# Kernel optimization log

Hardware: AMD Instinct MI355X
Metric: run time of the kernel (lower is better)

The kernel has to match this reference:

```python
import jax, jax.numpy as jnp
import numpy as np

N = 100000
E = 1600000
IN_DIM, HID_DIM, OUT_DIM = 128, 128, 64


def setup_inputs() -> dict:
    key = jax.random.key(0)
    k1, k2, k3, k4, k5, k6 = jax.random.split(key, 6)
    x = jax.random.normal(k1, (N, IN_DIM), dtype=jnp.float32)
    edge_index = jax.random.randint(k2, (2, E), 0, N, dtype=jnp.int64)
    # Glorot-style scaled weights (PyG GCNConv: Linear without bias + separate bias)
    W1 = jax.random.normal(k3, (IN_DIM, HID_DIM), dtype=jnp.float32) / np.sqrt(IN_DIM)
    b1 = jnp.zeros((HID_DIM,), dtype=jnp.float32)
    W2 = jax.random.normal(k4, (HID_DIM, OUT_DIM), dtype=jnp.float32) / np.sqrt(HID_DIM)
    b2 = jnp.zeros((OUT_DIM,), dtype=jnp.float32)
    return {"x": x, "W1": W1, "b1": b1, "W2": W2, "b2": b2, "edge_index": edge_index}


def _gcn_norm(edge_index, num_nodes):
    """Add self-loops and compute symmetric normalization D^-1/2 A_hat D^-1/2."""
    loop = jnp.arange(num_nodes, dtype=edge_index.dtype)
    src = jnp.concatenate([edge_index[0], loop])  # [E + N]
    dst = jnp.concatenate([edge_index[1], loop])
    deg = jax.ops.segment_sum(jnp.ones_like(dst, dtype=jnp.float32), dst,
                              num_segments=num_nodes)
    deg_inv_sqrt = jnp.where(deg > 0, jax.lax.rsqrt(deg), 0.0)
    norm = deg_inv_sqrt[src] * deg_inv_sqrt[dst]  # [E + N]
    return src, dst, norm


def _gcn_conv(x, W, b, src, dst, norm, num_nodes):
    h = x @ W                                   # [N, out]  dense transform first
    msg = norm[:, None] * h[src]                # gather + scale over edges
    out = jax.ops.segment_sum(msg, dst, num_segments=num_nodes)  # scatter-add
    return out + b


def reference(x, W1, b1, W2, b2, edge_index):
    num_nodes = x.shape[0]
    src, dst, norm = _gcn_norm(edge_index, num_nodes)
    h = jax.nn.relu(_gcn_conv(x, W1, b1, src, dst, norm, num_nodes))
    out = _gcn_conv(h, W2, b2, src, dst, norm, num_nodes)
    return out
```

## Files before the change

### kernel.cpp

```cpp
#include <hip/hip_runtime.h>

#define NODES 100000
#define EDGES 1600000
#define CHUNK 8192
#define NCH 196
#define BSH 9
#define NBUCK 196

typedef unsigned int uint;
typedef unsigned short ushort;

__device__ __forceinline__ float bf2f(uint u) {
    union { uint i; float f; } c; c.i = u << 16; return c.f;
}
__device__ __forceinline__ ushort f2bf(float f) {
    union { float f; uint i; } c; c.f = f;
    uint r = c.i + 0x7fff + ((c.i >> 16) & 1);
    return (ushort)(r >> 16);
}


__global__ __launch_bounds__(256) void k_hist(const int* __restrict__ dst,
                                              int* __restrict__ hist) {
    __shared__ int h[NBUCK];
    const int t = threadIdx.x;
    if (t < NBUCK) h[t] = 0;
    __syncthreads();
    const int base = blockIdx.x * CHUNK;
    const int len = min(CHUNK, EDGES - base);
    for (int i = t; i < len; i += 256)
        atomicAdd(&h[dst[base + i] >> BSH], 1);
    __syncthreads();
    if (t < NBUCK) hist[blockIdx.x * NBUCK + t] = h[t];
}

__global__ void k_offsets(int* __restrict__ hist, int* __restrict__ bucketStart,
                          int* __restrict__ rowptr) {
    __shared__ int tot[NBUCK];
    __shared__ int bstart[NBUCK + 1];
    const int t = threadIdx.x;
    if (t < NBUCK) {
        int run = 0;
        for (int blk = 0; blk < NCH; ++blk) {
            int c = hist[blk * NBUCK + t];
            hist[blk * NBUCK + t] = run;
            run += c;
        }
        tot[t] = run;
    }
    __syncthreads();
    if (t == 0) {
        int acc = 0;
        for (int b = 0; b < NBUCK; ++b) { bstart[b] = acc; acc += tot[b]; }
        bstart[NBUCK] = acc;
        rowptr[NODES] = acc;
    }
    __syncthreads();
    if (t < NBUCK) {
        int bs = bstart[t];
        for (int blk = 0; blk < NCH; ++blk)
            hist[blk * NBUCK + t] += bs;
    }
    if (t <= NBUCK) bucketStart[t] = bstart[t];
}

__global__ __launch_bounds__(256) void k_bin(const int* __restrict__ src,
                                             const int* __restrict__ dst,
                                             const int* __restrict__ hist,
                                             uint* __restrict__ binned) {
    __shared__ int curs[NBUCK];
    const int t = threadIdx.x;
    if (t < NBUCK) curs[t] = hist[blockIdx.x * NBUCK + t];
    __syncthreads();
    const int base = blockIdx.x * CHUNK;
    const int len = min(CHUNK, EDGES - base);
    for (int i = t; i < len; i += 256) {
        int d = dst[base + i];
        int s = src[base + i];
        int pos = atomicAdd(&curs[d >> BSH], 1);
        binned[pos] = ((uint)(d & 511) << 17) | (uint)s;
    }
}

__global__ __launch_bounds__(256) void k_build(const uint* __restrict__ binned,
                                               const int* __restrict__ bucketStart,
                                               int* __restrict__ rowptr,
                                               float* __restrict__ dis,
                                               int* __restrict__ ssrc) {
    __shared__ int cnt[512];
    __shared__ int sh[256];
    const int t = threadIdx.x;
    const int b = blockIdx.x;
    const int eBase = bucketStart[b], eEnd = bucketStart[b + 1];
    const int nodeBase = b << BSH;
    const int nnode = min(512, NODES - nodeBase);
    cnt[t * 2] = 0; cnt[t * 2 + 1] = 0;
    __syncthreads();
    for (int i = eBase + t; i < eEnd; i += 256)
        atomicAdd(&cnt[binned[i] >> 17], 1);
    __syncthreads();
    const int c0 = cnt[t * 2], c1 = cnt[t * 2 + 1];
    const int sum = c0 + c1;
    sh[t] = sum; __syncthreads();
    for (int off = 1; off < 256; off <<= 1) {
        int add = (t >= off) ? sh[t - off] : 0;
        __syncthreads(); sh[t] += add; __syncthreads();
    }
    int excl = sh[t] - sum;
    const int ln0 = t * 2;
    if (ln0 < nnode) {
        rowptr[nodeBase + ln0] = eBase + excl;
        dis[nodeBase + ln0] = rsqrtf((float)(1 + c0));
    }
    int excl1 = excl + c0;
    if (ln0 + 1 < nnode) {
        rowptr[nodeBase + ln0 + 1] = eBase + excl1;
        dis[nodeBase + ln0 + 1] = rsqrtf((float)(1 + c1));
    }
    cnt[ln0] = excl; cnt[ln0 + 1] = excl1;
    __syncthreads();
    for (int i = eBase + t; i < eEnd; i += 256) {
        uint p = binned[i];
        int pos = atomicAdd(&cnt[p >> 17], 1);
        ssrc[eBase + pos] = (int)(p & 0x1FFFFu);
    }
}


__global__ __launch_bounds__(256) void k_gemm1(const float* __restrict__ x,
                                               const float* __restrict__ W1,
                                               const float* __restrict__ dis,
                                               ushort* __restrict__ hb) {
    __shared__ float wsh[128 * 128];
    __shared__ float xs[32 * 128];
    const int t = threadIdx.x;
    {
        const float4* Wv = (const float4*)W1;
        float4* Sv = (float4*)wsh;
#pragma unroll
        for (int i = 0; i < 16; ++i) Sv[i * 256 + t] = Wv[i * 256 + t];
    }
    const int row0 = blockIdx.x * 32;
    {
        const float4* Xv = (const float4*)(x + (size_t)row0 * 128);
        float4* Sv = (float4*)xs;
#pragma unroll
        for (int i = 0; i < 4; ++i) Sv[i * 256 + t] = Xv[i * 256 + t];
    }
    __syncthreads();
    const int c4 = (t & 31) * 4;
    const int r0 = (t >> 5) * 4;
    float4 a0{0,0,0,0}, a1{0,0,0,0}, a2{0,0,0,0}, a3{0,0,0,0};
#pragma unroll 4
    for (int k = 0; k < 128; ++k) {
        float4 w = *(const float4*)&wsh[k * 128 + c4];
        float x0 = xs[(r0 + 0) * 128 + k];
        float x1 = xs[(r0 + 1) * 128 + k];
        float x2 = xs[(r0 + 2) * 128 + k];
        float x3 = xs[(r0 + 3) * 128 + k];
        a0.x = fmaf(x0, w.x, a0.x); a0.y = fmaf(x0, w.y, a0.y);
        a0.z = fmaf(x0, w.z, a0.z); a0.w = fmaf(x0, w.w, a0.w);
        a1.x = fmaf(x1, w.x, a1.x); a1.y = fmaf(x1, w.y, a1.y);
        a1.z = fmaf(x1, w.z, a1.z); a1.w = fmaf(x1, w.w, a1.w);
        a2.x = fmaf(x2, w.x, a2.x); a2.y = fmaf(x2, w.y, a2.y);
        a2.z = fmaf(x2, w.z, a2.z); a2.w = fmaf(x2, w.w, a2.w);
        a3.x = fmaf(x3, w.x, a3.x); a3.y = fmaf(x3, w.y, a3.y);
        a3.z = fmaf(x3, w.z, a3.z); a3.w = fmaf(x3, w.w, a3.w);
    }
    const float d0 = dis[row0 + r0], d1 = dis[row0 + r0 + 1];
    const float d2 = dis[row0 + r0 + 2], d3 = dis[row0 + r0 + 3];
    size_t base = (size_t)(row0 + r0) * 128 + c4;
    ushort4 u;
    u.x = f2bf(a0.x * d0); u.y = f2bf(a0.y * d0); u.z = f2bf(a0.z * d0); u.w = f2bf(a0.w * d0);
    *(ushort4*)&hb[base] = u;
    u.x = f2bf(a1.x * d1); u.y = f2bf(a1.y * d1); u.z = f2bf(a1.z * d1); u.w = f2bf(a1.w * d1);
    *(ushort4*)&hb[base + 128] = u;
    u.x = f2bf(a2.x * d2); u.y = f2bf(a2.y * d2); u.z = f2bf(a2.z * d2); u.w = f2bf(a2.w * d2);
    *(ushort4*)&hb[base + 256] = u;
    u.x = f2bf(a3.x * d3); u.y = f2bf(a3.y * d3); u.z = f2bf(a3.z * d3); u.w = f2bf(a3.w * d3);
    *(ushort4*)&hb[base + 384] = u;
}

__global__ __launch_bounds__(256) void k_gemm2(const uint* __restrict__ ab,
                                               const float* __restrict__ W2,
                                               const float* __restrict__ dis,
                                               ushort* __restrict__ gb) {
    __shared__ float wsh[128 * 64];
    __shared__ float xs[32 * 132];
    const int t = threadIdx.x;
    {
        const float4* Wv = (const float4*)W2;
        float4* Sv = (float4*)wsh;
#pragma unroll
        for (int i = 0; i < 8; ++i) Sv[i * 256 + t] = Wv[i * 256 + t];
    }
    const int row0 = blockIdx.x * 32;
    {
        const uint4* Xv = (const uint4*)(ab + (size_t)row0 * 64);
#pragma unroll
        for (int i = 0; i < 2; ++i) {
            int f = i * 256 + t;
            uint4 vv = Xv[f];
            int row = f >> 4, col = (f & 15) * 8;
            float* d = &xs[row * 132 + col];
            d[0] = bf2f(vv.x & 0xffffu); d[1] = bf2f(vv.x >> 16);
            d[2] = bf2f(vv.y & 0xffffu); d[3] = bf2f(vv.y >> 16);
            d[4] = bf2f(vv.z & 0xffffu); d[5] = bf2f(vv.z >> 16);
            d[6] = bf2f(vv.w & 0xffffu); d[7] = bf2f(vv.w >> 16);
        }
    }
    __syncthreads();
    const int c4 = (t & 15) * 4;
    const int r0 = (t >> 4) * 2;
    float4 a0{0,0,0,0}, a1{0,0,0,0};
#pragma unroll 4
    for (int k = 0; k < 128; ++k) {
        float4 w = *(const float4*)&wsh[k * 64 + c4];
        float x0 = xs[(r0 + 0) * 132 + k];
        float x1 = xs[(r0 + 1) * 132 + k];
        a0.x = fmaf(x0, w.x, a0.x); a0.y = fmaf(x0, w.y, a0.y);
        a0.z = fmaf(x0, w.z, a0.z); a0.w = fmaf(x0, w.w, a0.w);
        a1.x = fmaf(x1, w.x, a1.x); a1.y = fmaf(x1, w.y, a1.y);
        a1.z = fmaf(x1, w.z, a1.z); a1.w = fmaf(x1, w.w, a1.w);
    }
    const float d0 = dis[row0 + r0], d1 = dis[row0 + r0 + 1];
    size_t base = (size_t)(row0 + r0) * 64 + c4;
    ushort4 u;
    u.x = f2bf(a0.x * d0); u.y = f2bf(a0.y * d0); u.z = f2bf(a0.z * d0); u.w = f2bf(a0.w * d0);
    *(ushort4*)&gb[base] = u;
    u.x = f2bf(a1.x * d1); u.y = f2bf(a1.y * d1); u.z = f2bf(a1.z * d1); u.w = f2bf(a1.w * d1);
    *(ushort4*)&gb[base + 64] = u;
}


__global__ void k_agg1(const int* __restrict__ rowptr, const int* __restrict__ ssrc,
                       const float* __restrict__ dis, const uint2* __restrict__ hb2,
                       const float* __restrict__ b1, uint2* __restrict__ ab2) {
    const int t = threadIdx.x;
    const int lane = t & 63;
    const int q = lane & 31;
    const int v = blockIdx.x * 8 + ((t >> 6) << 1) + (lane >> 5);
    float4 accA, accB = {0.f, 0.f, 0.f, 0.f};
    {
        uint2 pv = hb2[(size_t)v * 32 + q];
        accA.x = bf2f(pv.x & 0xffffu); accA.y = bf2f(pv.x >> 16);
        accA.z = bf2f(pv.y & 0xffffu); accA.w = bf2f(pv.y >> 16);
    }
    int e = rowptr[v];
    const int end = rowptr[v + 1];
    while (e < end) {
        int m = end - e; if (m > 32) m = 32;
        int s = (q < m) ? ssrc[e + q] : 0;
        int i = 0;
        for (; i + 4 <= m; i += 4) {
            int s0 = __shfl(s, i + 0, 32);
            int s1 = __shfl(s, i + 1, 32);
            int s2 = __shfl(s, i + 2, 32);
            int s3 = __shfl(s, i + 3, 32);
            uint2 p0 = hb2[(size_t)s0 * 32 + q];
            uint2 p1 = hb2[(size_t)s1 * 32 + q];
            uint2 p2 = hb2[(size_t)s2 * 32 + q];
            uint2 p3 = hb2[(size_t)s3 * 32 + q];
            accA.x += bf2f(p0.x & 0xffffu); accA.y += bf2f(p0.x >> 16);
            accA.z += bf2f(p0.y & 0xffffu); accA.w += bf2f(p0.y >> 16);
            accB.x += bf2f(p1.x & 0xffffu); accB.y += bf2f(p1.x >> 16);
            accB.z += bf2f(p1.y & 0xffffu); accB.w += bf2f(p1.y >> 16);
            accA.x += bf2f(p2.x & 0xffffu); accA.y += bf2f(p2.x >> 16);
            accA.z += bf2f(p2.y & 0xffffu); accA.w += bf2f(p2.y >> 16);
            accB.x += bf2f(p3.x & 0xffffu); accB.y += bf2f(p3.x >> 16);
            accB.z += bf2f(p3.y & 0xffffu); accB.w += bf2f(p3.y >> 16);
        }
        for (; i < m; ++i) {
            int s0 = __shfl(s, i, 32);
            uint2 p0 = hb2[(size_t)s0 * 32 + q];
            accA.x += bf2f(p0.x & 0xffffu); accA.y += bf2f(p0.x >> 16);
            accA.z += bf2f(p0.y & 0xffffu); accA.w += bf2f(p0.y >> 16);
        }
        e += m;
    }
    const float dv = dis[v];
    const float4 bb = ((const float4*)b1)[q];
    float ox = fmaxf(fmaf(dv, accA.x + accB.x, bb.x), 0.f);
    float oy = fmaxf(fmaf(dv, accA.y + accB.y, bb.y), 0.f);
    float oz = fmaxf(fmaf(dv, accA.z + accB.z, bb.z), 0.f);
    float ow = fmaxf(fmaf(dv, accA.w + accB.w, bb.w), 0.f);
    uint2 o;
    o.x = ((uint)f2bf(oy) << 16) | (uint)f2bf(ox);
    o.y = ((uint)f2bf(ow) << 16) | (uint)f2bf(oz);
    ab2[(size_t)v * 32 + q] = o;
}

__global__ void k_agg2(const int* __restrict__ rowptr, const int* __restrict__ ssrc,
                       const float* __restrict__ dis, const uint* __restrict__ gbu,
                       const float* __restrict__ b2, float* __restrict__ out) {
    const int t = threadIdx.x;
    const int lane = t & 63;
    const int q = lane & 31;
    const int v = blockIdx.x * 8 + ((t >> 6) << 1) + (lane >> 5);
    float2 accA, accB = {0.f, 0.f};
    {
        uint pv = gbu[(size_t)v * 32 + q];
        accA.x = bf2f(pv & 0xffffu); accA.y = bf2f(pv >> 16);
    }
    int e = rowptr[v];
    const int end = rowptr[v + 1];
    while (e < end) {
        int m = end - e; if (m > 32) m = 32;
        int s = (q < m) ? ssrc[e + q] : 0;
        int i = 0;
        for (; i + 4 <= m; i += 4) {
            int s0 = __shfl(s, i + 0, 32);
            int s1 = __shfl(s, i + 1, 32);
            int s2 = __shfl(s, i + 2, 32);
            int s3 = __shfl(s, i + 3, 32);
            uint p0 = gbu[(size_t)s0 * 32 + q];
            uint p1 = gbu[(size_t)s1 * 32 + q];
            uint p2 = gbu[(size_t)s2 * 32 + q];
            uint p3 = gbu[(size_t)s3 * 32 + q];
            accA.x += bf2f(p0 & 0xffffu); accA.y += bf2f(p0 >> 16);
            accB.x += bf2f(p1 & 0xffffu); accB.y += bf2f(p1 >> 16);
            accA.x += bf2f(p2 & 0xffffu); accA.y += bf2f(p2 >> 16);
            accB.x += bf2f(p3 & 0xffffu); accB.y += bf2f(p3 >> 16);
        }
        for (; i < m; ++i) {
            int s0 = __shfl(s, i, 32);
            uint p0 = gbu[(size_t)s0 * 32 + q];
            accA.x += bf2f(p0 & 0xffffu); accA.y += bf2f(p0 >> 16);
        }
        e += m;
    }
    const float dv = dis[v];
    const float2 bb = ((const float2*)b2)[q];
    float2 o;
    o.x = fmaf(dv, accA.x + accB.x, bb.x);
    o.y = fmaf(dv, accA.y + accB.y, bb.y);
    ((float2*)out)[(size_t)v * 32 + q] = o;
}


extern "C" void kernel_launch(void* const* d_in, const int* in_sizes, int n_in,
                              void* d_out, int out_size, void* d_ws, size_t ws_size,
                              hipStream_t stream) {
    const float* x  = (const float*)d_in[0];
    const float* W1 = (const float*)d_in[1];
    const float* b1 = (const float*)d_in[2];
    const float* W2 = (const float*)d_in[3];
    const float* b2 = (const float*)d_in[4];
    const int*   ei = (const int*)d_in[5];
    const int* src = ei;
    const int* dst = ei + EDGES;
    float* out = (float*)d_out;

    char* w = (char*)d_ws;
    int*    hist   = (int*)w;    w += (size_t)NCH * NBUCK * 4 + 256;
    int*    bstart = (int*)w;    w += 256 * 4;
    int*    rowptr = (int*)w;    w += 100004 * 4;
    float*  dis    = (float*)w;  w += 100000 * 4 + 16;
    uint*   binned = (uint*)w;   w += (size_t)EDGES * 4;
    int*    ssrc   = (int*)w;    w += (size_t)EDGES * 4;
    ushort* hb     = (ushort*)w; w += (size_t)NODES * 128 * 2;
    uint*   ab     = (uint*)w;   w += (size_t)NODES * 64 * 4;
    ushort* gb     = (ushort*)w; w += (size_t)NODES * 64 * 2;

    k_hist   <<<NCH, 256, 0, stream>>>(dst, hist);
    k_offsets<<<1, 256, 0, stream>>>(hist, bstart, rowptr);
    k_bin    <<<NCH, 256, 0, stream>>>(src, dst, hist, binned);
    k_build  <<<NBUCK, 256, 0, stream>>>(binned, bstart, rowptr, dis, ssrc);

    k_gemm1  <<<NODES / 32, 256, 0, stream>>>(x, W1, dis, hb);
    k_agg1   <<<NODES / 8, 256, 0, stream>>>(rowptr, ssrc, dis, (const uint2*)hb, b1, (uint2*)ab);
    k_gemm2  <<<NODES / 32, 256, 0, stream>>>(ab, W2, dis, gb);
    k_agg2   <<<NODES / 8, 256, 0, stream>>>(rowptr, ssrc, dis, (const uint*)gb, b2, out);
}
```

Before: 386.0 us.

## Split aggregation feature dimension across blocks for cache locality

Both aggregation kernels now run as grid-stride loops in which each block owns a fixed slice of the feature dimension: 16 features in layer 1, 8 in layer 2. Each wave handles one node at a time, with several edge slots in flight; partial sums are combined by a cross-lane xor-shuffle reduction and one lane group writes the result. The aim is to shrink the per-block gather working set to one slice of the feature table so it stays in L2, and to have more independent edge gathers in flight per wave. The cost is that rowptr and ssrc are re-read once per feature slice, and each gather is a narrow 32- or 16-byte segment rather than a full row.

```diff
diff --git a/kernel.cpp b/kernel.cpp
--- a/kernel.cpp
+++ b/kernel.cpp
@@ -6,6 +6,7 @@
 #define NCH 196
 #define BSH 9
 #define NBUCK 196
+#define NGRP (NODES / 4)
 
 typedef unsigned int uint;
 typedef unsigned short ushort;
@@ -233,108 +234,92 @@
 }
 
 
-__global__ void k_agg1(const int* __restrict__ rowptr, const int* __restrict__ ssrc,
-                       const float* __restrict__ dis, const uint2* __restrict__ hb2,
-                       const float* __restrict__ b1, uint2* __restrict__ ab2) {
-    const int t = threadIdx.x;
+__global__ __launch_bounds__(256) void k_agg1(const int* __restrict__ rowptr,
+                                              const int* __restrict__ ssrc,
+                                              const float* __restrict__ dis,
+                                              const uint* __restrict__ hbu,
+                                              const float* __restrict__ b1,
+                                              uint* __restrict__ abu) {
+    const int t = threadIdx.x;
+    const int wave = t >> 6;
     const int lane = t & 63;
-    const int q = lane & 31;
-    const int v = blockIdx.x * 8 + ((t >> 6) << 1) + (lane >> 5);
-    float4 accA, accB = {0.f, 0.f, 0.f, 0.f};
-    {
-        uint2 pv = hb2[(size_t)v * 32 + q];
-        accA.x = bf2f(pv.x & 0xffffu); accA.y = bf2f(pv.x >> 16);
-        accA.z = bf2f(pv.y & 0xffffu); accA.w = bf2f(pv.y >> 16);
-    }
-    int e = rowptr[v];
-    const int end = rowptr[v + 1];
-    while (e < end) {
-        int m = end - e; if (m > 32) m = 32;
-        int s = (q < m) ? ssrc[e + q] : 0;
-        int i = 0;
-        for (; i + 4 <= m; i += 4) {
-            int s0 = __shfl(s, i + 0, 32);
-            int s1 = __shfl(s, i + 1, 32);
-            int s2 = __shfl(s, i + 2, 32);
-            int s3 = __shfl(s, i + 3, 32);
-            uint2 p0 = hb2[(size_t)s0 * 32 + q];
-            uint2 p1 = hb2[(size_t)s1 * 32 + q];
-            uint2 p2 = hb2[(size_t)s2 * 32 + q];
-            uint2 p3 = hb2[(size_t)s3 * 32 + q];
-            accA.x += bf2f(p0.x & 0xffffu); accA.y += bf2f(p0.x >> 16);
-            accA.z += bf2f(p0.y & 0xffffu); accA.w += bf2f(p0.y >> 16);
-            accB.x += bf2f(p1.x & 0xffffu); accB.y += bf2f(p1.x >> 16);
-            accB.z += bf2f(p1.y & 0xffffu); accB.w += bf2f(p1.y >> 16);
-            accA.x += bf2f(p2.x & 0xffffu); accA.y += bf2f(p2.x >> 16);
-            accA.z += bf2f(p2.y & 0xffffu); accA.w += bf2f(p2.y >> 16);
-            accB.x += bf2f(p3.x & 0xffffu); accB.y += bf2f(p3.x >> 16);
-            accB.z += bf2f(p3.y & 0xffffu); accB.w += bf2f(p3.y >> 16);
-        }
-        for (; i < m; ++i) {
-            int s0 = __shfl(s, i, 32);
-            uint2 p0 = hb2[(size_t)s0 * 32 + q];
-            accA.x += bf2f(p0.x & 0xffffu); accA.y += bf2f(p0.x >> 16);
-            accA.z += bf2f(p0.y & 0xffffu); accA.w += bf2f(p0.y >> 16);
-        }
-        e += m;
-    }
-    const float dv = dis[v];
-    const float4 bb = ((const float4*)b1)[q];
-    float ox = fmaxf(fmaf(dv, accA.x + accB.x, bb.x), 0.f);
-    float oy = fmaxf(fmaf(dv, accA.y + accB.y, bb.y), 0.f);
-    float oz = fmaxf(fmaf(dv, accA.z + accB.z, bb.z), 0.f);
-    float ow = fmaxf(fmaf(dv, accA.w + accB.w, bb.w), 0.f);
-    uint2 o;
-    o.x = ((uint)f2bf(oy) << 16) | (uint)f2bf(ox);
-    o.y = ((uint)f2bf(ow) << 16) | (uint)f2bf(oz);
-    ab2[(size_t)v * 32 + q] = o;
-}
-
-__global__ void k_agg2(const int* __restrict__ rowptr, const int* __restrict__ ssrc,
-                       const float* __restrict__ dis, const uint* __restrict__ gbu,
-                       const float* __restrict__ b2, float* __restrict__ out) {
-    const int t = threadIdx.x;
+    const int slot = lane >> 3;
+    const int d = lane & 7;
+    const int chunk = blockIdx.x & 7;
+    const int base = chunk * 8 + d;
+    const int ngroups = gridDim.x >> 3;
+    for (int group = blockIdx.x >> 3; group < NGRP; group += ngroups) {
+        const int v = group * 4 + wave;
+        float ax = 0.f, ay = 0.f;
+        const int end = rowptr[v + 1];
+        for (int e = rowptr[v]; e < end; e += 8) {
+            int idx = e + slot;
+            if (idx < end) {
+                int s = ssrc[idx];
+                uint p = hbu[(size_t)s * 64 + base];
+                ax += bf2f(p & 0xffffu);
+                ay += bf2f(p >> 16);
+            }
+        }
+        ax += __shfl_xor(ax, 8);  ay += __shfl_xor(ay, 8);
+        ax += __shfl_xor(ax, 16); ay += __shfl_xor(ay, 16);
+        ax += __shfl_xor(ax, 32); ay += __shfl_xor(ay, 32);
+        if (slot == 0) {
+            uint pv = hbu[(size_t)v * 64 + base];
+            float tx = ax + bf2f(pv & 0xffffu);
+            float ty = ay + bf2f(pv >> 16);
+            const float dv = dis[v];
+            const float2 bb = ((const float2*)b1)[base];
+            float ox = fmaxf(fmaf(dv, tx, bb.x), 0.f);
+            float oy = fmaxf(fmaf(dv, ty, bb.y), 0.f);
+            abu[(size_t)v * 64 + base] = ((uint)f2bf(oy) << 16) | (uint)f2bf(ox);
+        }
+    }
+}
+
+__global__ __launch_bounds__(256) void k_agg2(const int* __restrict__ rowptr,
+                                              const int* __restrict__ ssrc,
+                                              const float* __restrict__ dis,
+                                              const uint* __restrict__ gbu,
+                                              const float* __restrict__ b2,
+                                              float* __restrict__ out) {
+    const int t = threadIdx.x;
+    const int wave = t >> 6;
     const int lane = t & 63;
-    const int q = lane & 31;
-    const int v = blockIdx.x * 8 + ((t >> 6) << 1) + (lane >> 5);
-    float2 accA, accB = {0.f, 0.f};
-    {
-        uint pv = gbu[(size_t)v * 32 + q];
-        accA.x = bf2f(pv & 0xffffu); accA.y = bf2f(pv >> 16);
-    }
-    int e = rowptr[v];
-    const int end = rowptr[v + 1];
-    while (e < end) {
-        int m = end - e; if (m > 32) m = 32;
-        int s = (q < m) ? ssrc[e + q] : 0;
-        int i = 0;
-        for (; i + 4 <= m; i += 4) {
-            int s0 = __shfl(s, i + 0, 32);
-            int s1 = __shfl(s, i + 1, 32);
-            int s2 = __shfl(s, i + 2, 32);
-            int s3 = __shfl(s, i + 3, 32);
-            uint p0 = gbu[(size_t)s0 * 32 + q];
-            uint p1 = gbu[(size_t)s1 * 32 + q];
-            uint p2 = gbu[(size_t)s2 * 32 + q];
-            uint p3 = gbu[(size_t)s3 * 32 + q];
-            accA.x += bf2f(p0 & 0xffffu); accA.y += bf2f(p0 >> 16);
-            accB.x += bf2f(p1 & 0xffffu); accB.y += bf2f(p1 >> 16);
-            accA.x += bf2f(p2 & 0xffffu); accA.y += bf2f(p2 >> 16);
-            accB.x += bf2f(p3 & 0xffffu); accB.y += bf2f(p3 >> 16);
-        }
-        for (; i < m; ++i) {
-            int s0 = __shfl(s, i, 32);
-            uint p0 = gbu[(size_t)s0 * 32 + q];
-            accA.x += bf2f(p0 & 0xffffu); accA.y += bf2f(p0 >> 16);
-        }
-        e += m;
-    }
-    const float dv = dis[v];
-    const float2 bb = ((const float2*)b2)[q];
-    float2 o;
-    o.x = fmaf(dv, accA.x + accB.x, bb.x);
-    o.y = fmaf(dv, accA.y + accB.y, bb.y);
-    ((float2*)out)[(size_t)v * 32 + q] = o;
+    const int slot = lane >> 2;
+    const int d = lane & 3;
+    const int chunk = blockIdx.x & 7;
+    const int base = chunk * 4 + d;
+    const int ngroups = gridDim.x >> 3;
+    for (int group = blockIdx.x >> 3; group < NGRP; group += ngroups) {
+        const int v = group * 4 + wave;
+        float ax = 0.f, ay = 0.f;
+        const int end = rowptr[v + 1];
+        for (int e = rowptr[v]; e < end; e += 16) {
+            int idx = e + slot;
+            if (idx < end) {
+                int s = ssrc[idx];
+                uint p = gbu[(size_t)s * 32 + base];
+                ax += bf2f(p & 0xffffu);
+                ay += bf2f(p >> 16);
+            }
+        }
+        ax += __shfl_xor(ax, 4);  ay += __shfl_xor(ay, 4);
+        ax += __shfl_xor(ax, 8);  ay += __shfl_xor(ay, 8);
+        ax += __shfl_xor(ax, 16); ay += __shfl_xor(ay, 16);
+        ax += __shfl_xor(ax, 32); ay += __shfl_xor(ay, 32);
+        if (slot == 0) {
+            uint pv = gbu[(size_t)v * 32 + base];
+            float tx = ax + bf2f(pv & 0xffffu);
+            float ty = ay + bf2f(pv >> 16);
+            const float dv = dis[v];
+            const float2 bb = ((const float2*)b2)[base];
+            float2 o;
+            o.x = fmaf(dv, tx, bb.x);
+            o.y = fmaf(dv, ty, bb.y);
+            ((float2*)out)[(size_t)v * 32 + base] = o;
+        }
+    }
 }
 
 
@@ -368,7 +353,7 @@
     k_build  <<<NBUCK, 256, 0, stream>>>(binned, bstart, rowptr, dis, ssrc);
 
     k_gemm1  <<<NODES / 32, 256, 0, stream>>>(x, W1, dis, hb);
-    k_agg1   <<<NODES / 8, 256, 0, stream>>>(rowptr, ssrc, dis, (const uint2*)hb, b1, (uint2*)ab);
-    k_gemm2  <<<NODES / 32, 256, 0, stream>>>(ab, W2, dis, gb);
-    k_agg2   <<<NODES / 8, 256, 0, stream>>>(rowptr, ssrc, dis, (const uint*)gb, b2, out);
-}
+    k_agg1   <<<16384, 256, 0, stream>>>(rowptr, ssrc, dis, (const uint*)hb, b1, (uint*)ab);
+    k_gemm2  <<<NODES / 32, 256, 0, stream>>>((const uint*)ab, W2, dis, gb);
+    k_agg2   <<<16384, 256, 0, stream>>>(rowptr, ssrc, dis, (const uint*)gb, b2, out);
+}
```

After: 731.9 us. 1.9x slower.

## Use bf16 MFMA for both GEMMs and transpose histogram layout for prefix scan

Applied to the files above, without the earlier changes.

Both dense transforms now run on matrix cores: a small kernel converts W1 and W2 to transposed bf16, and the GEMM kernels stage x (converted to bf16) and the activations in padded shared memory, then use 16x16x32 bf16 MFMA with 64-row tiles. The aim is to replace the scalar-FMA fp32 GEMMs, which carry heavy shared-memory traffic and a large W tile. The bucket histogram is stored bucket-major so each thread scans a contiguous row, and a parallel scan replaces the serial single-thread bucket prefix. Converting x to bf16 loses input precision, and the output stores are scalar 2-byte scattered writes.

```diff
diff --git a/kernel.cpp b/kernel.cpp
--- a/kernel.cpp
+++ b/kernel.cpp
@@ -9,6 +9,8 @@
 
 typedef unsigned int uint;
 typedef unsigned short ushort;
+typedef __attribute__((ext_vector_type(8))) short bf16x8;
+typedef __attribute__((ext_vector_type(4))) float f32x4;
 
 __device__ __forceinline__ float bf2f(uint u) {
     union { uint i; float f; } c; c.i = u << 16; return c.f;
@@ -31,37 +33,33 @@
     for (int i = t; i < len; i += 256)
         atomicAdd(&h[dst[base + i] >> BSH], 1);
     __syncthreads();
-    if (t < NBUCK) hist[blockIdx.x * NBUCK + t] = h[t];
+    if (t < NBUCK) hist[t * NCH + blockIdx.x] = h[t];
 }
 
 __global__ void k_offsets(int* __restrict__ hist, int* __restrict__ bucketStart,
                           int* __restrict__ rowptr) {
-    __shared__ int tot[NBUCK];
-    __shared__ int bstart[NBUCK + 1];
-    const int t = threadIdx.x;
+    __shared__ int sh[256];
+    const int t = threadIdx.x;
+    int run = 0;
     if (t < NBUCK) {
-        int run = 0;
+        int* rowp = hist + (size_t)t * NCH;
         for (int blk = 0; blk < NCH; ++blk) {
-            int c = hist[blk * NBUCK + t];
-            hist[blk * NBUCK + t] = run;
-            run += c;
-        }
-        tot[t] = run;
-    }
-    __syncthreads();
-    if (t == 0) {
-        int acc = 0;
-        for (int b = 0; b < NBUCK; ++b) { bstart[b] = acc; acc += tot[b]; }
-        bstart[NBUCK] = acc;
-        rowptr[NODES] = acc;
-    }
-    __syncthreads();
+            int c = rowp[blk]; rowp[blk] = run; run += c;
+        }
+    }
+    int v = (t < NBUCK) ? run : 0;
+    sh[t] = v; __syncthreads();
+    for (int off = 1; off < 256; off <<= 1) {
+        int add = (t >= off) ? sh[t - off] : 0;
+        __syncthreads(); sh[t] += add; __syncthreads();
+    }
+    int excl = sh[t] - v;
     if (t < NBUCK) {
-        int bs = bstart[t];
-        for (int blk = 0; blk < NCH; ++blk)
-            hist[blk * NBUCK + t] += bs;
-    }
-    if (t <= NBUCK) bucketStart[t] = bstart[t];
+        bucketStart[t] = excl;
+        int* rowp = hist + (size_t)t * NCH;
+        for (int blk = 0; blk < NCH; ++blk) rowp[blk] += excl;
+    }
+    if (t == 255) { bucketStart[NBUCK] = sh[255]; rowptr[NODES] = sh[255]; }
 }
 
 __global__ __launch_bounds__(256) void k_bin(const int* __restrict__ src,
@@ -70,7 +68,7 @@
                                              uint* __restrict__ binned) {
     __shared__ int curs[NBUCK];
     const int t = threadIdx.x;
-    if (t < NBUCK) curs[t] = hist[blockIdx.x * NBUCK + t];
+    if (t < NBUCK) curs[t] = hist[t * NCH + blockIdx.x];
     __syncthreads();
     const int base = blockIdx.x * CHUNK;
     const int len = min(CHUNK, EDGES - base);
@@ -127,109 +125,140 @@
 }
 
 
+__global__ void k_prepW(const float* __restrict__ W1, const float* __restrict__ W2,
+                        ushort* __restrict__ W1t, ushort* __restrict__ W2t) {
+    const int t = threadIdx.x + blockIdx.x * 256;
+    for (int i = t; i < 128 * 128; i += 512) {
+        int n = i >> 7, k = i & 127;
+        W1t[i] = f2bf(W1[k * 128 + n]);
+    }
+    for (int i = t; i < 64 * 128; i += 512) {
+        int n = i >> 7, k = i & 127;
+        W2t[i] = f2bf(W2[k * 64 + n]);
+    }
+}
+
+
 __global__ __launch_bounds__(256) void k_gemm1(const float* __restrict__ x,
-                                               const float* __restrict__ W1,
+                                               const ushort* __restrict__ W1t,
                                                const float* __restrict__ dis,
                                                ushort* __restrict__ hb) {
-    __shared__ float wsh[128 * 128];
-    __shared__ float xs[32 * 128];
-    const int t = threadIdx.x;
-    {
-        const float4* Wv = (const float4*)W1;
-        float4* Sv = (float4*)wsh;
-#pragma unroll
-        for (int i = 0; i < 16; ++i) Sv[i * 256 + t] = Wv[i * 256 + t];
-    }
-    const int row0 = blockIdx.x * 32;
-    {
-        const float4* Xv = (const float4*)(x + (size_t)row0 * 128);
-        float4* Sv = (float4*)xs;
-#pragma unroll
-        for (int i = 0; i < 4; ++i) Sv[i * 256 + t] = Xv[i * 256 + t];
-    }
-    __syncthreads();
-    const int c4 = (t & 31) * 4;
-    const int r0 = (t >> 5) * 4;
-    float4 a0{0,0,0,0}, a1{0,0,0,0}, a2{0,0,0,0}, a3{0,0,0,0};
-#pragma unroll 4
-    for (int k = 0; k < 128; ++k) {
-        float4 w = *(const float4*)&wsh[k * 128 + c4];
-        float x0 = xs[(r0 + 0) * 128 + k];
-        float x1 = xs[(r0 + 1) * 128 + k];
-        float x2 = xs[(r0 + 2) * 128 + k];
-        float x3 = xs[(r0 + 3) * 128 + k];
-        a0.x = fmaf(x0, w.x, a0.x); a0.y = fmaf(x0, w.y, a0.y);
-        a0.z = fmaf(x0, w.z, a0.z); a0.w = fmaf(x0, w.w, a0.w);
-        a1.x = fmaf(x1, w.x, a1.x); a1.y = fmaf(x1, w.y, a1.y);
-        a1.z = fmaf(x1, w.z, a1.z); a1.w = fmaf(x1, w.w, a1.w);
-        a2.x = fmaf(x2, w.x, a2.x); a2.y = fmaf(x2, w.y, a2.y);
-        a2.z = fmaf(x2, w.z, a2.z); a2.w = fmaf(x2, w.w, a2.w);
-        a3.x = fmaf(x3, w.x, a3.x); a3.y = fmaf(x3, w.y, a3.y);
-        a3.z = fmaf(x3, w.z, a3.z); a3.w = fmaf(x3, w.w, a3.w);
-    }
-    const float d0 = dis[row0 + r0], d1 = dis[row0 + r0 + 1];
-    const float d2 = dis[row0 + r0 + 2], d3 = dis[row0 + r0 + 3];
-    size_t base = (size_t)(row0 + r0) * 128 + c4;
-    ushort4 u;
-    u.x = f2bf(a0.x * d0); u.y = f2bf(a0.y * d0); u.z = f2bf(a0.z * d0); u.w = f2bf(a0.w * d0);
-    *(ushort4*)&hb[base] = u;
-    u.x = f2bf(a1.x * d1); u.y = f2bf(a1.y * d1); u.z = f2bf(a1.z * d1); u.w = f2bf(a1.w * d1);
-    *(ushort4*)&hb[base + 128] = u;
-    u.x = f2bf(a2.x * d2); u.y = f2bf(a2.y * d2); u.z = f2bf(a2.z * d2); u.w = f2bf(a2.w * d2);
-    *(ushort4*)&hb[base + 256] = u;
-    u.x = f2bf(a3.x * d3); u.y = f2bf(a3.y * d3); u.z = f2bf(a3.z * d3); u.w = f2bf(a3.w * d3);
-    *(ushort4*)&hb[base + 384] = u;
+    __shared__ __align__(16) ushort wt[128 * 136];
+    __shared__ __align__(16) ushort xs[64 * 136];
+    const int t = threadIdx.x;
+    const int wave = t >> 6;
+    const int lane = t & 63;
+    const int row0 = blockIdx.x * 64;
+    {
+        const uint4* Wg = (const uint4*)W1t;
+#pragma unroll
+        for (int i = 0; i < 8; ++i) {
+            int flat = i * 256 + t;
+            int n = flat >> 4, c = flat & 15;
+            *(uint4*)&wt[n * 136 + c * 8] = Wg[flat];
+        }
+    }
+    {
+#pragma unroll
+        for (int i = 0; i < 16; ++i) {
+            int flat = i * 256 + t;
+            int r = flat >> 6, cp = flat & 63;
+            int row = row0 + r; if (row >= NODES) row = NODES - 1;
+            float2 v = *(const float2*)&x[(size_t)row * 128 + cp * 2];
+            *(uint*)&xs[r * 136 + cp * 2] = ((uint)f2bf(v.y) << 16) | (uint)f2bf(v.x);
+        }
+    }
+    __syncthreads();
+    const int arow = lane & 15;
+    const int kg = (lane >> 4) * 8;
+    f32x4 acc[8] = {};
+#pragma unroll
+    for (int ks = 0; ks < 4; ++ks) {
+        const int k0 = ks * 32;
+        bf16x8 a = *(const bf16x8*)&xs[(wave * 16 + arow) * 136 + k0 + kg];
+#pragma unroll
+        for (int nt = 0; nt < 8; ++nt) {
+            bf16x8 b = *(const bf16x8*)&wt[(nt * 16 + arow) * 136 + k0 + kg];
+            acc[nt] = __builtin_amdgcn_mfma_f32_16x16x32_bf16(a, b, acc[nt], 0, 0, 0);
+        }
+    }
+    const int m4 = (lane >> 4) * 4;
+    int nodes[4]; float dv[4];
+#pragma unroll
+    for (int r = 0; r < 4; ++r) {
+        int node = row0 + wave * 16 + m4 + r;
+        nodes[r] = node;
+        dv[r] = dis[node < NODES ? node : NODES - 1];
+    }
+#pragma unroll
+    for (int nt = 0; nt < 8; ++nt) {
+#pragma unroll
+        for (int r = 0; r < 4; ++r) {
+            if (nodes[r] < NODES)
+                hb[(size_t)nodes[r] * 128 + nt * 16 + (lane & 15)] = f2bf(acc[nt][r] * dv[r]);
+        }
+    }
 }
 
 __global__ __launch_bounds__(256) void k_gemm2(const uint* __restrict__ ab,
-                                               const float* __restrict__ W2,
+                                               const ushort* __restrict__ W2t,
                                                const float* __restrict__ dis,
                                                ushort* __restrict__ gb) {
-    __shared__ float wsh[128 * 64];
-    __shared__ float xs[32 * 132];
-    const int t = threadIdx.x;
-    {
-        const float4* Wv = (const float4*)W2;
-        float4* Sv = (float4*)wsh;
-#pragma unroll
-        for (int i = 0; i < 8; ++i) Sv[i * 256 + t] = Wv[i * 256 + t];
-    }
-    const int row0 = blockIdx.x * 32;
-    {
-        const uint4* Xv = (const uint4*)(ab + (size_t)row0 * 64);
-#pragma unroll
-        for (int i = 0; i < 2; ++i) {
-            int f = i * 256 + t;
-            uint4 vv = Xv[f];
-            int row = f >> 4, col = (f & 15) * 8;
-            float* d = &xs[row * 132 + col];
-            d[0] = bf2f(vv.x & 0xffffu); d[1] = bf2f(vv.x >> 16);
-            d[2] = bf2f(vv.y & 0xffffu); d[3] = bf2f(vv.y >> 16);
-            d[4] = bf2f(vv.z & 0xffffu); d[5] = bf2f(vv.z >> 16);
-            d[6] = bf2f(vv.w & 0xffffu); d[7] = bf2f(vv.w >> 16);
-        }
-    }
-    __syncthreads();
-    const int c4 = (t & 15) * 4;
-    const int r0 = (t >> 4) * 2;
-    float4 a0{0,0,0,0}, a1{0,0,0,0};
-#pragma unroll 4
-    for (int k = 0; k < 128; ++k) {
-        float4 w = *(const float4*)&wsh[k * 64 + c4];
-        float x0 = xs[(r0 + 0) * 132 + k];
-        float x1 = xs[(r0 + 1) * 132 + k];
-        a0.x = fmaf(x0, w.x, a0.x); a0.y = fmaf(x0, w.y, a0.y);
-        a0.z = fmaf(x0, w.z, a0.z); a0.w = fmaf(x0, w.w, a0.w);
-        a1.x = fmaf(x1, w.x, a1.x); a1.y = fmaf(x1, w.y, a1.y);
-        a1.z = fmaf(x1, w.z, a1.z); a1.w = fmaf(x1, w.w, a1.w);
-    }
-    const float d0 = dis[row0 + r0], d1 = dis[row0 + r0 + 1];
-    size_t base = (size_t)(row0 + r0) * 64 + c4;
-    ushort4 u;
-    u.x = f2bf(a0.x * d0); u.y = f2bf(a0.y * d0); u.z = f2bf(a0.z * d0); u.w = f2bf(a0.w * d0);
-    *(ushort4*)&gb[base] = u;
-    u.x = f2bf(a1.x * d1); u.y = f2bf(a1.y * d1); u.z = f2bf(a1.z * d1); u.w = f2bf(a1.w * d1);
-    *(ushort4*)&gb[base + 64] = u;
+    __shared__ __align__(16) ushort wt[64 * 136];
+    __shared__ __align__(16) ushort xs[64 * 136];
+    const int t = threadIdx.x;
+    const int wave = t >> 6;
+    const int lane = t & 63;
+    const int row0 = blockIdx.x * 64;
+    {
+        const uint4* Wg = (const uint4*)W2t;
+#pragma unroll
+        for (int i = 0; i < 4; ++i) {
+            int flat = i * 256 + t;
+            int n = flat >> 4, c = flat & 15;
+            *(uint4*)&wt[n * 136 + c * 8] = Wg[flat];
+        }
+    }
+    {
+        const uint4* Ag = (const uint4*)ab;
+#pragma unroll
+        for (int i = 0; i < 4; ++i) {
+            int flat = i * 256 + t;
+            int r = flat >> 4, c = flat & 15;
+            int row = row0 + r; if (row >= NODES) row = NODES - 1;
+            *(uint4*)&xs[r * 136 + c * 8] = Ag[(size_t)row * 16 + c];
+        }
+    }
+    __syncthreads();
+    const int arow = lane & 15;
+    const int kg = (lane >> 4) * 8;
+    f32x4 acc[4] = {};
+#pragma unroll
+    for (int ks = 0; ks < 4; ++ks) {
+        const int k0 = ks * 32;
+        bf16x8 a = *(const bf16x8*)&xs[(wave * 16 + arow) * 136 + k0 + kg];
+#pragma unroll
+        for (int nt = 0; nt < 4; ++nt) {
+            bf16x8 b = *(const bf16x8*)&wt[(nt * 16 + arow) * 136 + k0 + kg];
+            acc[nt] = __builtin_amdgcn_mfma_f32_16x16x32_bf16(a, b, acc[nt], 0, 0, 0);
+        }
+    }
+    const int m4 = (lane >> 4) * 4;
+    int nodes[4]; float dv[4];
+#pragma unroll
+    for (int r = 0; r < 4; ++r) {
+        int node = row0 + wave * 16 + m4 + r;
+        nodes[r] = node;
+        dv[r] = dis[node < NODES ? node : NODES - 1];
+    }
+#pragma unroll
+    for (int nt = 0; nt < 4; ++nt) {
+#pragma unroll
+        for (int r = 0; r < 4; ++r) {
+            if (nodes[r] < NODES)
+                gb[(size_t)nodes[r] * 64 + nt * 16 + (lane & 15)] = f2bf(acc[nt][r] * dv[r]);
+        }
+    }
 }
 
 
@@ -361,14 +390,17 @@
     ushort* hb     = (ushort*)w; w += (size_t)NODES * 128 * 2;
     uint*   ab     = (uint*)w;   w += (size_t)NODES * 64 * 4;
     ushort* gb     = (ushort*)w; w += (size_t)NODES * 64 * 2;
-
+    ushort* W1t    = (ushort*)w; w += 128 * 128 * 2;
+    ushort* W2t    = (ushort*)w; w += 64 * 128 * 2;
+
+    k_prepW  <<<2, 256, 0, stream>>>(W1, W2, W1t, W2t);
     k_hist   <<<NCH, 256, 0, stream>>>(dst, hist);
     k_offsets<<<1, 256, 0, stream>>>(hist, bstart, rowptr);
     k_bin    <<<NCH, 256, 0, stream>>>(src, dst, hist, binned);
     k_build  <<<NBUCK, 256, 0, stream>>>(binned, bstart, rowptr, dis, ssrc);
 
-    k_gemm1  <<<NODES / 32, 256, 0, stream>>>(x, W1, dis, hb);
+    k_gemm1  <<<(NODES + 63) / 64, 256, 0, stream>>>(x, W1t, dis, hb);
     k_agg1   <<<NODES / 8, 256, 0, stream>>>(rowptr, ssrc, dis, (const uint2*)hb, b1, (uint2*)ab);
-    k_gemm2  <<<NODES / 32, 256, 0, stream>>>(ab, W2, dis, gb);
+    k_gemm2  <<<(NODES + 63) / 64, 256, 0, stream>>>((const uint*)ab, W2t, dis, gb);
     k_agg2   <<<NODES / 8, 256, 0, stream>>>(rowptr, ssrc, dis, (const uint*)gb, b2, out);
 }
```

Result: faster. 330.4 us (-14.4%).
